# Performance work log

Measured on AMD Instinct MI355X. Metric: run time of the kernel, lower is better.

Reference implementation:

```python
import jax, jax.numpy as jnp
import numpy as np

USER_COUNT = 100000
ITEM_COUNT = 50000
N_NODES = USER_COUNT + ITEM_COUNT
NNZ = 4800000
EMB = 64
BATCH = 4096


def setup_inputs() -> dict:
    key = jax.random.key(0)
    k1, k2, k3, k4, k5, k6, k7 = jax.random.split(key, 7)
    return {
        "user_emb": jax.random.normal(k1, (USER_COUNT, EMB), dtype=jnp.float32),
        "item_emb": jax.random.normal(k2, (ITEM_COUNT, EMB), dtype=jnp.float32),
        "adj_vals": jax.random.uniform(k3, (NNZ,), dtype=jnp.float32),
        "adj_row": jax.random.randint(k4, (NNZ,), 0, N_NODES, dtype=jnp.int64),
        "adj_col": jax.random.randint(k5, (NNZ,), 0, N_NODES, dtype=jnp.int64),
        "users": jax.random.randint(k6, (BATCH,), 0, USER_COUNT, dtype=jnp.int64),
        "items": jax.random.randint(k7, (BATCH,), 0, ITEM_COUNT, dtype=jnp.int64),
        "n_layers": 3,
    }


def _spmm(adj_row, adj_col, adj_vals, x):
    # sparse (N,N) @ dense (N,D): gather source rows, scale by edge values, scatter-add to dest
    msgs = adj_vals[:, None] * x[adj_col]  # [nnz, D]
    return jax.ops.segment_sum(msgs, adj_row, num_segments=N_NODES)


def reference(user_emb, item_emb, adj_vals, adj_row, adj_col, users, items, n_layers):
    ego = jnp.concatenate([user_emb, item_emb], axis=0)  # [N, D]
    for _ in range(n_layers):
        ego = _spmm(adj_row, adj_col, adj_vals, ego)
    user_all = ego[:USER_COUNT]
    item_all = ego[USER_COUNT:]
    return (user_all[users], item_all[items])
```

## Files before the change

### kernel.cpp

```cpp
#include <hip/hip_runtime.h>
#include <hip/hip_bf16.h>

#define USER_COUNT 100000
#define ITEM_COUNT 50000
#define N_NODES    150000
#define EMB        64
#define BATCH      4096

#define NFINE      586
#define FSHIFT     8
#define CAP        13
#define STRIDE     8960
#define P1_BLOCKS  512
#define P1_THREADS 512
#define TILE       1024
#define OVF_CAP    4096

__device__ inline unsigned short f2bf_raw(float f) {
    __hip_bfloat16 h = __float2bfloat16(f);
    unsigned short u; __builtin_memcpy(&u, &h, 2); return u;
}

__global__ __launch_bounds__(P1_THREADS) void partition_kernel(
        const float* __restrict__ vals,
        const int* __restrict__ rows,
        const int* __restrict__ cols,
        uint2* __restrict__ fine,
        int*   __restrict__ gcur,
        uint4* __restrict__ ovf,
        int*   __restrict__ ovf_cnt,
        int nnz) {
    __shared__ uint2 stage[NFINE * CAP];
    __shared__ int   cnt[NFINE];
    const int tid = threadIdx.x;
    for (int f = tid; f < NFINE; f += P1_THREADS) cnt[f] = 0;
    __syncthreads();

    const int per   = (nnz + P1_BLOCKS - 1) / P1_BLOCKS;
    const int start = blockIdx.x * per;
    const int stop  = min(start + per, nnz);

    for (int tbase = start; tbase < stop; tbase += TILE) {
        #pragma unroll
        for (int k = 0; k < 2; ++k) {
            int i = tbase + k * P1_THREADS + tid;
            if (i < stop) {
                int r = rows[i];
                int f = r >> FSHIFT;
                uint2 e;
                e.x = __float_as_uint(vals[i]);
                e.y = (unsigned)cols[i] | ((unsigned)(r & 255) << 18);
                int slot = atomicAdd(&cnt[f], 1);
                if (slot < CAP) {
                    stage[f * CAP + slot] = e;
                } else {
                    int p = atomicAdd(ovf_cnt, 1);
                    if (p < OVF_CAP)
                        ovf[p] = make_uint4(e.x, (unsigned)cols[i], (unsigned)r, 0u);
                }
            }
        }
        __syncthreads();
        for (int f = tid; f < NFINE; f += P1_THREADS) {
            int n = min(cnt[f], CAP);
            int nfull = n & ~7;
            if (nfull > 0) {
                int b = atomicAdd(&gcur[f], nfull);
                uint2* dst = fine + (size_t)f * STRIDE + b;
                for (int k = 0; k < nfull; ++k) dst[k] = stage[f * CAP + k];
                for (int k = nfull; k < n; ++k)
                    stage[f * CAP + (k - nfull)] = stage[f * CAP + k];
            }
            cnt[f] = n - nfull;
        }
        __syncthreads();
    }
    for (int f = tid; f < NFINE; f += P1_THREADS) {
        int n = min(cnt[f], CAP);
        if (n > 0) {
            int b = atomicAdd(&gcur[f], n);
            uint2* dst = fine + (size_t)f * STRIDE + b;
            for (int k = 0; k < n; ++k) dst[k] = stage[f * CAP + k];
        }
    }
}

__global__ void ovf_fix_kernel(const uint4* __restrict__ ovf,
                               const int* __restrict__ ovf_cnt,
                               uint2* __restrict__ fine,
                               int* __restrict__ gcur) {
    int n = min(*ovf_cnt, OVF_CAP);
    for (int k = threadIdx.x; k < n; k += blockDim.x) {
        uint4 e = ovf[k];
        int f = (int)(e.z >> FSHIFT);
        int pos = atomicAdd(&gcur[f], 1);
        fine[(size_t)f * STRIDE + pos] = make_uint2(e.x, e.y | ((e.z & 255u) << 18));
    }
}

__global__ void scan_fbase_kernel(const int* __restrict__ gcur,
                                  int* __restrict__ fbase) {
    if (threadIdx.x == 0) {
        int acc = 0;
        for (int f = 0; f < NFINE; ++f) { fbase[f] = acc; acc += gcur[f]; }
    }
}

__global__ __launch_bounds__(256) void bucket_sort_kernel(
        const uint2* __restrict__ fine,
        const int* __restrict__ gcur,
        const int* __restrict__ fbase,
        float2* __restrict__ perm,
        int* __restrict__ row_ptr) {
    __shared__ int hist[256];
    __shared__ int off[256];
    __shared__ int cur[256];
    const int f   = blockIdx.x;
    const int tid = threadIdx.x;
    const int n   = gcur[f];
    const int fb  = fbase[f];
    const uint2* src = fine + (size_t)f * STRIDE;

    hist[tid] = 0;
    __syncthreads();
    for (int k = tid; k < n; k += 256)
        atomicAdd(&hist[(src[k].y >> 18) & 255], 1);
    __syncthreads();
    if (tid == 0) {
        int acc = 0;
        for (int j = 0; j < 256; ++j) { off[j] = acc; acc += hist[j]; }
    }
    __syncthreads();
    cur[tid] = off[tid];
    int row = (f << FSHIFT) + tid;
    if (row <= N_NODES) row_ptr[row] = fb + off[tid];
    __syncthreads();
    for (int k = tid; k < n; k += 256) {
        uint2 e = src[k];
        int lrow = (e.y >> 18) & 255;
        int pos = fb + atomicAdd(&cur[lrow], 1);
        perm[pos] = make_float2(__uint_as_float(e.x),
                                __int_as_float((int)(e.y & 0x3FFFFu)));
    }
}

__global__ void to_bf16(const float4* __restrict__ ue,
                        const float4* __restrict__ ie,
                        uint2* __restrict__ xh) {
    int i = blockIdx.x * blockDim.x + threadIdx.x;
    const int n4 = (N_NODES * EMB) / 4;
    const int u4 = (USER_COUNT * EMB) / 4;
    if (i >= n4) return;
    float4 fv = (i < u4) ? ue[i] : ie[i - u4];
    uint2 o;
    o.x = (unsigned int)f2bf_raw(fv.x) | ((unsigned int)f2bf_raw(fv.y) << 16);
    o.y = (unsigned int)f2bf_raw(fv.z) | ((unsigned int)f2bf_raw(fv.w) << 16);
    xh[i] = o;
}

__global__ void spmm_bf16(const int* __restrict__ row_ptr,
                          const float2* __restrict__ perm,
                          const unsigned short* __restrict__ xh,
                          unsigned short* __restrict__ yh) {
    int wid  = (blockIdx.x * blockDim.x + threadIdx.x) >> 6;
    int lane = threadIdx.x & 63;
    int g    = lane >> 4;
    int s    = lane & 15;
    int r    = (wid << 2) + g;
    if (r >= N_NODES) return;

    int beg = row_ptr[r];
    int end = row_ptr[r + 1];

    const uint2* xv = (const uint2*)xh;
    float ax = 0.f, ay = 0.f, az = 0.f, aw = 0.f;

    int j = beg;
    for (; j + 3 < end; j += 4) {
        float2 e0 = perm[j];
        float2 e1 = perm[j + 1];
        float2 e2 = perm[j + 2];
        float2 e3 = perm[j + 3];
        uint2 u0 = xv[(((long long)__float_as_int(e0.y)) << 4) + s];
        uint2 u1 = xv[(((long long)__float_as_int(e1.y)) << 4) + s];
        uint2 u2 = xv[(((long long)__float_as_int(e2.y)) << 4) + s];
        uint2 u3 = xv[(((long long)__float_as_int(e3.y)) << 4) + s];
        ax += e0.x * __uint_as_float(u0.x << 16);
        ay += e0.x * __uint_as_float(u0.x & 0xffff0000u);
        az += e0.x * __uint_as_float(u0.y << 16);
        aw += e0.x * __uint_as_float(u0.y & 0xffff0000u);
        ax += e1.x * __uint_as_float(u1.x << 16);
        ay += e1.x * __uint_as_float(u1.x & 0xffff0000u);
        az += e1.x * __uint_as_float(u1.y << 16);
        aw += e1.x * __uint_as_float(u1.y & 0xffff0000u);
        ax += e2.x * __uint_as_float(u2.x << 16);
        ay += e2.x * __uint_as_float(u2.x & 0xffff0000u);
        az += e2.x * __uint_as_float(u2.y << 16);
        aw += e2.x * __uint_as_float(u2.y & 0xffff0000u);
        ax += e3.x * __uint_as_float(u3.x << 16);
        ay += e3.x * __uint_as_float(u3.x & 0xffff0000u);
        az += e3.x * __uint_as_float(u3.y << 16);
        aw += e3.x * __uint_as_float(u3.y & 0xffff0000u);
    }
    for (; j < end; ++j) {
        float2 e = perm[j];
        uint2 u = xv[(((long long)__float_as_int(e.y)) << 4) + s];
        ax += e.x * __uint_as_float(u.x << 16);
        ay += e.x * __uint_as_float(u.x & 0xffff0000u);
        az += e.x * __uint_as_float(u.y << 16);
        aw += e.x * __uint_as_float(u.y & 0xffff0000u);
    }

    uint2 o;
    o.x = (unsigned int)f2bf_raw(ax) | ((unsigned int)f2bf_raw(ay) << 16);
    o.y = (unsigned int)f2bf_raw(az) | ((unsigned int)f2bf_raw(aw) << 16);
    ((uint2*)yh)[(((long long)r) << 4) + s] = o;
}

__global__ void spmm_batch_kernel(const int* __restrict__ row_ptr,
                                  const float2* __restrict__ perm,
                                  const unsigned short* __restrict__ xh,
                                  const int* __restrict__ users,
                                  const int* __restrict__ items,
                                  float4* __restrict__ out) {
    int wid  = (blockIdx.x * blockDim.x + threadIdx.x) >> 6;
    int lane = threadIdx.x & 63;
    int g    = lane >> 4;
    int s    = lane & 15;
    int b    = (wid << 2) + g;
    if (b >= 2 * BATCH) return;
    int node = (b < BATCH) ? users[b] : (USER_COUNT + items[b - BATCH]);

    int beg = row_ptr[node];
    int end = row_ptr[node + 1];

    const uint2* xv = (const uint2*)xh;
    float ax = 0.f, ay = 0.f, az = 0.f, aw = 0.f;

    int j = beg;
    for (; j + 3 < end; j += 4) {
        float2 e0 = perm[j];
        float2 e1 = perm[j + 1];
        float2 e2 = perm[j + 2];
        float2 e3 = perm[j + 3];
        uint2 u0 = xv[(((long long)__float_as_int(e0.y)) << 4) + s];
        uint2 u1 = xv[(((long long)__float_as_int(e1.y)) << 4) + s];
        uint2 u2 = xv[(((long long)__float_as_int(e2.y)) << 4) + s];
        uint2 u3 = xv[(((long long)__float_as_int(e3.y)) << 4) + s];
        ax += e0.x * __uint_as_float(u0.x << 16);
        ay += e0.x * __uint_as_float(u0.x & 0xffff0000u);
        az += e0.x * __uint_as_float(u0.y << 16);
        aw += e0.x * __uint_as_float(u0.y & 0xffff0000u);
        ax += e1.x * __uint_as_float(u1.x << 16);
        ay += e1.x * __uint_as_float(u1.x & 0xffff0000u);
        az += e1.x * __uint_as_float(u1.y << 16);
        aw += e1.x * __uint_as_float(u1.y & 0xffff0000u);
        ax += e2.x * __uint_as_float(u2.x << 16);
        ay += e2.x * __uint_as_float(u2.x & 0xffff0000u);
        az += e2.x * __uint_as_float(u2.y << 16);
        aw += e2.x * __uint_as_float(u2.y & 0xffff0000u);
        ax += e3.x * __uint_as_float(u3.x << 16);
        ay += e3.x * __uint_as_float(u3.x & 0xffff0000u);
        az += e3.x * __uint_as_float(u3.y << 16);
        aw += e3.x * __uint_as_float(u3.y & 0xffff0000u);
    }
    for (; j < end; ++j) {
        float2 e = perm[j];
        uint2 u = xv[(((long long)__float_as_int(e.y)) << 4) + s];
        ax += e.x * __uint_as_float(u.x << 16);
        ay += e.x * __uint_as_float(u.x & 0xffff0000u);
        az += e.x * __uint_as_float(u.y << 16);
        aw += e.x * __uint_as_float(u.y & 0xffff0000u);
    }

    out[(size_t)b * 16 + s] = make_float4(ax, ay, az, aw);
}

extern "C" void kernel_launch(void* const* d_in, const int* in_sizes, int n_in,
                              void* d_out, int out_size, void* d_ws, size_t ws_size,
                              hipStream_t stream) {
    const float* user_emb = (const float*)d_in[0];
    const float* item_emb = (const float*)d_in[1];
    const float* adj_vals = (const float*)d_in[2];
    const int*   adj_row  = (const int*)d_in[3];
    const int*   adj_col  = (const int*)d_in[4];
    const int*   users    = (const int*)d_in[5];
    const int*   items    = (const int*)d_in[6];

    const int nnz = in_sizes[2];

    char* p = (char*)d_ws;
    uint2* fine = (uint2*)p;
    unsigned short* xh_a = (unsigned short*)p;
    unsigned short* xh_b = xh_a + (size_t)N_NODES * EMB;
    p += (size_t)NFINE * STRIDE * sizeof(uint2);
    float2* perm = (float2*)p;
    p += ((size_t)nnz + OVF_CAP) * sizeof(float2);
    int* row_ptr = (int*)p;
    p += (size_t)(N_NODES + 16) * sizeof(int);
    int* gcur = (int*)p;       p += NFINE * sizeof(int);
    int* fbase = (int*)p;      p += NFINE * sizeof(int);
    int* ovf_cnt = (int*)p;    p += 16 * sizeof(int);
    uint4* ovf = (uint4*)p;

    hipMemsetAsync(gcur, 0, (NFINE + 16 + NFINE) * sizeof(int), stream);
    partition_kernel<<<P1_BLOCKS, P1_THREADS, 0, stream>>>(
        adj_vals, adj_row, adj_col, fine, gcur, ovf, ovf_cnt, nnz);
    ovf_fix_kernel<<<1, 256, 0, stream>>>(ovf, ovf_cnt, fine, gcur);
    scan_fbase_kernel<<<1, 64, 0, stream>>>(gcur, fbase);
    bucket_sort_kernel<<<NFINE, 256, 0, stream>>>(fine, gcur, fbase, perm, row_ptr);

    const int n4 = (N_NODES * EMB) / 4;
    to_bf16<<<(n4 + 255) / 256, 256, 0, stream>>>((const float4*)user_emb,
                                                  (const float4*)item_emb,
                                                  (uint2*)xh_a);

    const int spmm_blocks = (N_NODES / 4 + 3) / 4;
    spmm_bf16<<<spmm_blocks, 256, 0, stream>>>(row_ptr, perm, xh_a, xh_b);
    spmm_bf16<<<spmm_blocks, 256, 0, stream>>>(row_ptr, perm, xh_b, xh_a);
    spmm_batch_kernel<<<(2 * BATCH / 4 + 3) / 4, 256, 0, stream>>>(
        row_ptr, perm, xh_a, users, items, (float4*)d_out);
}
```

Baseline: 480.2 us.

## Replace staged partition with count-scan-scatter two-pass partition

Replaces the single-pass partition, which staged edges in shared memory, flushed them to fixed-stride buckets and sent spills to an overflow buffer, with a deterministic counting sort. Per-block bucket counts are computed first, then reduced and scanned into exact offsets, and edges are scattered straight into a compact array. This removes the overflow path, the global atomics and the padded bucket layout. The cost is an extra full read of the row indices, four extra small kernel launches, and scattered 8-byte writes in place of the staged batches of 8.

```diff
diff --git a/kernel.cpp b/kernel.cpp
--- a/kernel.cpp
+++ b/kernel.cpp
@@ -9,106 +9,91 @@
 
 #define NFINE      586
 #define FSHIFT     8
-#define CAP        13
-#define STRIDE     8960
-#define P1_BLOCKS  512
-#define P1_THREADS 512
-#define TILE       1024
-#define OVF_CAP    4096
+#define NBLK_P     512
+#define PTHREADS   512
 
 __device__ inline unsigned short f2bf_raw(float f) {
     __hip_bfloat16 h = __float2bfloat16(f);
     unsigned short u; __builtin_memcpy(&u, &h, 2); return u;
 }
 
-__global__ __launch_bounds__(P1_THREADS) void partition_kernel(
+__global__ __launch_bounds__(PTHREADS) void count_kernel(
+        const int* __restrict__ rows, int* __restrict__ counts, int nnz) {
+    __shared__ int cnt[NFINE];
+    const int b = blockIdx.x, t = threadIdx.x;
+    for (int f = t; f < NFINE; f += PTHREADS) cnt[f] = 0;
+    __syncthreads();
+    const int per = (nnz + NBLK_P - 1) / NBLK_P;
+    const int s = b * per, e = min(s + per, nnz);
+    for (int i = s + t; i < e; i += PTHREADS)
+        atomicAdd(&cnt[rows[i] >> FSHIFT], 1);
+    __syncthreads();
+    for (int f = t; f < NFINE; f += PTHREADS)
+        counts[f * NBLK_P + b] = cnt[f];
+}
+
+__global__ __launch_bounds__(NBLK_P) void reduce_tot(
+        const int* __restrict__ counts, int* __restrict__ tot) {
+    __shared__ int red[NBLK_P];
+    const int f = blockIdx.x, t = threadIdx.x;
+    red[t] = counts[f * NBLK_P + t];
+    __syncthreads();
+    for (int o = NBLK_P / 2; o > 0; o >>= 1) {
+        if (t < o) red[t] += red[t + o];
+        __syncthreads();
+    }
+    if (t == 0) tot[f] = red[0];
+}
+
+__global__ void scan_fbase_kernel(const int* __restrict__ tot,
+                                  int* __restrict__ fbase) {
+    if (threadIdx.x == 0) {
+        int acc = 0;
+        for (int f = 0; f < NFINE; ++f) { fbase[f] = acc; acc += tot[f]; }
+    }
+}
+
+__global__ __launch_bounds__(NBLK_P) void scan_offs(
+        const int* __restrict__ counts, const int* __restrict__ fbase,
+        int* __restrict__ offs) {
+    __shared__ int s[NBLK_P];
+    const int f = blockIdx.x, t = threadIdx.x;
+    const int c = counts[f * NBLK_P + t];
+    s[t] = c;
+    __syncthreads();
+    for (int o = 1; o < NBLK_P; o <<= 1) {
+        int v = (t >= o) ? s[t - o] : 0;
+        __syncthreads();
+        s[t] += v;
+        __syncthreads();
+    }
+    offs[f * NBLK_P + t] = fbase[f] + s[t] - c;
+}
+
+__global__ __launch_bounds__(PTHREADS) void partition_kernel(
         const float* __restrict__ vals,
         const int* __restrict__ rows,
         const int* __restrict__ cols,
-        uint2* __restrict__ fine,
-        int*   __restrict__ gcur,
-        uint4* __restrict__ ovf,
-        int*   __restrict__ ovf_cnt,
-        int nnz) {
-    __shared__ uint2 stage[NFINE * CAP];
-    __shared__ int   cnt[NFINE];
-    const int tid = threadIdx.x;
-    for (int f = tid; f < NFINE; f += P1_THREADS) cnt[f] = 0;
-    __syncthreads();
-
-    const int per   = (nnz + P1_BLOCKS - 1) / P1_BLOCKS;
-    const int start = blockIdx.x * per;
-    const int stop  = min(start + per, nnz);
-
-    for (int tbase = start; tbase < stop; tbase += TILE) {
-        #pragma unroll
-        for (int k = 0; k < 2; ++k) {
-            int i = tbase + k * P1_THREADS + tid;
-            if (i < stop) {
-                int r = rows[i];
-                int f = r >> FSHIFT;
-                uint2 e;
-                e.x = __float_as_uint(vals[i]);
-                e.y = (unsigned)cols[i] | ((unsigned)(r & 255) << 18);
-                int slot = atomicAdd(&cnt[f], 1);
-                if (slot < CAP) {
-                    stage[f * CAP + slot] = e;
-                } else {
-                    int p = atomicAdd(ovf_cnt, 1);
-                    if (p < OVF_CAP)
-                        ovf[p] = make_uint4(e.x, (unsigned)cols[i], (unsigned)r, 0u);
-                }
-            }
-        }
-        __syncthreads();
-        for (int f = tid; f < NFINE; f += P1_THREADS) {
-            int n = min(cnt[f], CAP);
-            int nfull = n & ~7;
-            if (nfull > 0) {
-                int b = atomicAdd(&gcur[f], nfull);
-                uint2* dst = fine + (size_t)f * STRIDE + b;
-                for (int k = 0; k < nfull; ++k) dst[k] = stage[f * CAP + k];
-                for (int k = nfull; k < n; ++k)
-                    stage[f * CAP + (k - nfull)] = stage[f * CAP + k];
-            }
-            cnt[f] = n - nfull;
-        }
-        __syncthreads();
-    }
-    for (int f = tid; f < NFINE; f += P1_THREADS) {
-        int n = min(cnt[f], CAP);
-        if (n > 0) {
-            int b = atomicAdd(&gcur[f], n);
-            uint2* dst = fine + (size_t)f * STRIDE + b;
-            for (int k = 0; k < n; ++k) dst[k] = stage[f * CAP + k];
-        }
-    }
-}
-
-__global__ void ovf_fix_kernel(const uint4* __restrict__ ovf,
-                               const int* __restrict__ ovf_cnt,
-                               uint2* __restrict__ fine,
-                               int* __restrict__ gcur) {
-    int n = min(*ovf_cnt, OVF_CAP);
-    for (int k = threadIdx.x; k < n; k += blockDim.x) {
-        uint4 e = ovf[k];
-        int f = (int)(e.z >> FSHIFT);
-        int pos = atomicAdd(&gcur[f], 1);
-        fine[(size_t)f * STRIDE + pos] = make_uint2(e.x, e.y | ((e.z & 255u) << 18));
-    }
-}
-
-__global__ void scan_fbase_kernel(const int* __restrict__ gcur,
-                                  int* __restrict__ fbase) {
-    if (threadIdx.x == 0) {
-        int acc = 0;
-        for (int f = 0; f < NFINE; ++f) { fbase[f] = acc; acc += gcur[f]; }
+        const int* __restrict__ offs,
+        uint2* __restrict__ fine, int nnz) {
+    __shared__ int cur[NFINE];
+    const int b = blockIdx.x, t = threadIdx.x;
+    for (int f = t; f < NFINE; f += PTHREADS) cur[f] = offs[f * NBLK_P + b];
+    __syncthreads();
+    const int per = (nnz + NBLK_P - 1) / NBLK_P;
+    const int s = b * per, e = min(s + per, nnz);
+    for (int i = s + t; i < e; i += PTHREADS) {
+        int r = rows[i];
+        int f = r >> FSHIFT;
+        int pos = atomicAdd(&cur[f], 1);
+        fine[pos] = make_uint2(__float_as_uint(vals[i]),
+                               (unsigned)cols[i] | ((unsigned)(r & 255) << 18));
     }
 }
 
 __global__ __launch_bounds__(256) void bucket_sort_kernel(
         const uint2* __restrict__ fine,
-        const int* __restrict__ gcur,
+        const int* __restrict__ tot,
         const int* __restrict__ fbase,
         float2* __restrict__ perm,
         int* __restrict__ row_ptr) {
@@ -117,9 +102,9 @@
     __shared__ int cur[256];
     const int f   = blockIdx.x;
     const int tid = threadIdx.x;
-    const int n   = gcur[f];
+    const int n   = tot[f];
     const int fb  = fbase[f];
-    const uint2* src = fine + (size_t)f * STRIDE;
+    const uint2* src = fine + fb;
 
     hist[tid] = 0;
     __syncthreads();
@@ -293,22 +278,23 @@
     uint2* fine = (uint2*)p;
     unsigned short* xh_a = (unsigned short*)p;
     unsigned short* xh_b = xh_a + (size_t)N_NODES * EMB;
-    p += (size_t)NFINE * STRIDE * sizeof(uint2);
+    p += (size_t)nnz * sizeof(uint2);
     float2* perm = (float2*)p;
-    p += ((size_t)nnz + OVF_CAP) * sizeof(float2);
+    p += (size_t)nnz * sizeof(float2);
     int* row_ptr = (int*)p;
     p += (size_t)(N_NODES + 16) * sizeof(int);
-    int* gcur = (int*)p;       p += NFINE * sizeof(int);
-    int* fbase = (int*)p;      p += NFINE * sizeof(int);
-    int* ovf_cnt = (int*)p;    p += 16 * sizeof(int);
-    uint4* ovf = (uint4*)p;
-
-    hipMemsetAsync(gcur, 0, (NFINE + 16 + NFINE) * sizeof(int), stream);
-    partition_kernel<<<P1_BLOCKS, P1_THREADS, 0, stream>>>(
-        adj_vals, adj_row, adj_col, fine, gcur, ovf, ovf_cnt, nnz);
-    ovf_fix_kernel<<<1, 256, 0, stream>>>(ovf, ovf_cnt, fine, gcur);
-    scan_fbase_kernel<<<1, 64, 0, stream>>>(gcur, fbase);
-    bucket_sort_kernel<<<NFINE, 256, 0, stream>>>(fine, gcur, fbase, perm, row_ptr);
+    int* counts = (int*)p;  p += (size_t)NFINE * NBLK_P * sizeof(int);
+    int* offs   = (int*)p;  p += (size_t)NFINE * NBLK_P * sizeof(int);
+    int* tot    = (int*)p;  p += (size_t)NFINE * sizeof(int);
+    int* fbase  = (int*)p;
+
+    count_kernel<<<NBLK_P, PTHREADS, 0, stream>>>(adj_row, counts, nnz);
+    reduce_tot<<<NFINE, NBLK_P, 0, stream>>>(counts, tot);
+    scan_fbase_kernel<<<1, 64, 0, stream>>>(tot, fbase);
+    scan_offs<<<NFINE, NBLK_P, 0, stream>>>(counts, fbase, offs);
+    partition_kernel<<<NBLK_P, PTHREADS, 0, stream>>>(adj_vals, adj_row, adj_col,
+                                                      offs, fine, nnz);
+    bucket_sort_kernel<<<NFINE, 256, 0, stream>>>(fine, tot, fbase, perm, row_ptr);
 
     const int n4 = (N_NODES * EMB) / 4;
     to_bf16<<<(n4 + 255) / 256, 256, 0, stream>>>((const float4*)user_emb,
```

Result: slower. 504.7 us (+5.1%).
